# Optimization experiments

Measured on AMD Instinct MI355X. Metric: run time of the kernel, lower is better.

## Reference

```python
import jax, jax.numpy as jnp
import numpy as np

LN_EPS = 1e-5

def _proj(x, w, b):
    # 1x1 conv: x [B,C,H,W], w [O,C], b [O]
    return jnp.einsum('bchw,oc->bohw', x, w) + b[None, :, None, None]

def _layernorm(x, w, b):
    # normalize over last dim
    mu = jnp.mean(x, axis=-1, keepdims=True)
    var = jnp.mean(jnp.square(x - mu), axis=-1, keepdims=True)
    return (x - mu) * jax.lax.rsqrt(var + LN_EPS) * w + b

def setup_inputs() -> dict:
    key = jax.random.key(0)
    ks = jax.random.split(key, 12)
    C = 256
    d = {
        's3': jax.random.normal(ks[0], (2, C, 64, 64), jnp.float32),
        's4': jax.random.normal(ks[1], (2, C, 32, 64), jnp.float32),
        's5': jax.random.normal(ks[2], (2, C, 16, 64), jnp.float32),
        'qw': jax.random.normal(ks[3], (C, C), jnp.float32) * 0.02,
        'qb': jax.random.normal(ks[4], (C,), jnp.float32) * 0.02,
        'kw': jax.random.normal(ks[5], (C, C), jnp.float32) * 0.02,
        'kb': jax.random.normal(ks[6], (C,), jnp.float32) * 0.02,
        'vw': jax.random.normal(ks[7], (C, C), jnp.float32) * 0.02,
        'vb': jax.random.normal(ks[8], (C,), jnp.float32) * 0.02,
        'ow': jax.random.normal(ks[9], (C, C), jnp.float32) * 0.02,
        'ob': jax.random.normal(ks[10], (C,), jnp.float32) * 0.02,
        'ln_w': jnp.ones((C,), jnp.float32),
        'ln_b': jnp.zeros((C,), jnp.float32),
    }
    return d

def reference(s3, s4, s5, qw, qb, kw, kb, vw, vb, ow, ob, ln_w, ln_b):
    B, C, H, W = s3.shape
    num_heads = 8
    head_dim = C // num_heads
    scale = head_dim ** -0.5

    q = _proj(s3, qw, qb).reshape(B, C, H * W)            # [B,C,Nq]
    k4 = _proj(s4, kw, kb).reshape(B, C, -1)
    k5 = _proj(s5, kw, kb).reshape(B, C, -1)
    v4 = _proj(s4, vw, vb).reshape(B, C, -1)
    v5 = _proj(s5, vw, vb).reshape(B, C, -1)
    k = jnp.concatenate([k4, k5], axis=-1)                # [B,C,Nk]
    v = jnp.concatenate([v4, v5], axis=-1)

    # [B,C,N] -> [B,h,N,d]
    def split_heads(t):
        Bn, Cn, N = t.shape
        return t.transpose(0, 2, 1).reshape(Bn, N, num_heads, head_dim).transpose(0, 2, 1, 3)

    qh, kh, vh = split_heads(q), split_heads(k), split_heads(v)
    attn = jnp.einsum('bhqd,bhkd->bhqk', qh, kh) * scale
    attn = jax.nn.softmax(attn, axis=-1)
    out = jnp.einsum('bhqk,bhkd->bhqd', attn, vh)         # [B,h,Nq,d]
    out = out.transpose(0, 2, 1, 3).reshape(B, H * W, C)  # [B,Nq,C]
    out = out.transpose(0, 2, 1).reshape(B, C, H, W)
    out = _proj(out, ow, ob)
    out = s3 + out
    out_flat = out.reshape(B, C, H * W).transpose(0, 2, 1)  # [B,N,C]
    out_flat = _layernorm(out_flat, ln_w, ln_b)
    return out_flat.transpose(0, 2, 1).reshape(B, C, H, W)
```

## Files before the change

kernel.cpp:

```cpp
#include <hip/hip_runtime.h>

typedef __bf16 bf16;
typedef __bf16 bf16x4 __attribute__((ext_vector_type(4)));
typedef __bf16 bf16x8 __attribute__((ext_vector_type(8)));
typedef _Float16 f16;
typedef _Float16 f16x2 __attribute__((ext_vector_type(2)));
typedef _Float16 f16x4 __attribute__((ext_vector_type(4)));
typedef _Float16 f16x8 __attribute__((ext_vector_type(8)));
typedef float f32x4 __attribute__((ext_vector_type(4)));
typedef unsigned int u32x4 __attribute__((ext_vector_type(4)));

#define MFMA16 __builtin_amdgcn_mfma_f32_16x16x32_bf16
#define MFMA16H __builtin_amdgcn_mfma_f32_16x16x32_f16

__device__ __forceinline__ void async16(void* lds, const void* g) {
    __builtin_amdgcn_global_load_lds((const __attribute__((address_space(1))) unsigned int*)g,
                                     (__attribute__((address_space(3))) unsigned int*)lds, 16, 0, 0);
}

__device__ __forceinline__ f16x2 pkrtz(float a, float b) {
    return __builtin_bit_cast(f16x2, __builtin_amdgcn_cvt_pkrtz(a, b));
}

__device__ __forceinline__ float fdot2h(f16x2 a, f16x2 b, float c) {
#if __has_builtin(__builtin_amdgcn_fdot2)
    return __builtin_amdgcn_fdot2(a, b, c, false);
#else
    return c + (float)a[0] * (float)b[0] + (float)a[1] * (float)b[1];
#endif
}

__global__ __launch_bounds__(256) void k_prep(const float* __restrict__ qw, const float* __restrict__ kw,
                                              const float* __restrict__ vw, const float* __restrict__ ow,
                                              bf16* __restrict__ Wb,
                                              const float* __restrict__ s3, const float* __restrict__ s4,
                                              const float* __restrict__ s5,
                                              bf16* __restrict__ s3t, bf16* __restrict__ s45t) {
    __shared__ float T[64][65];
    int bx = blockIdx.x, t = threadIdx.x;
    if (bx < 256) {
        int tt = bx * 256 + t;
        const float* srcs[4] = {qw, kw, vw, ow};
        int which = tt >> 14;
        int idx = (tt & 16383) * 4;
        f32x4 v = *(const f32x4*)(srcs[which] + idx);
        bf16x4 o;
        o[0] = (bf16)v[0]; o[1] = (bf16)v[1]; o[2] = (bf16)v[2]; o[3] = (bf16)v[3];
        *(bf16x4*)(Wb + (size_t)which * 65536 + idx) = o;
        return;
    }
    const float* src; bf16* dst; int N, dstRows, rowOff, x, y, z;
    if (bx < 768)       { int i = bx - 256;  src = s3; dst = s3t;  N = 4096; dstRows = 4096; rowOff = 0;    x = i & 63; y = (i >> 6) & 3; z = i >> 8; }
    else if (bx < 1024) { int i = bx - 768;  src = s4; dst = s45t; N = 2048; dstRows = 3072; rowOff = 0;    x = i & 31; y = (i >> 5) & 3; z = i >> 7; }
    else                { int i = bx - 1024; src = s5; dst = s45t; N = 1024; dstRows = 3072; rowOff = 2048; x = i & 15; y = (i >> 4) & 3; z = i >> 6; }
    int c0 = y * 64, n0 = x * 64, b = z;
    const float* s = src + ((size_t)b * 256 + c0) * N + n0;
#pragma unroll
    for (int i = 0; i < 4; i++) {
        int flat = i * 256 + t;
        int row = flat >> 4;
        int col = (flat & 15) * 4;
        f32x4 v = *(const f32x4*)(s + (size_t)row * N + col);
        T[row][col + 0] = v[0]; T[row][col + 1] = v[1];
        T[row][col + 2] = v[2]; T[row][col + 3] = v[3];
    }
    __syncthreads();
#pragma unroll
    for (int i = 0; i < 4; i++) {
        int flat = i * 256 + t;
        int nrow = flat >> 4;
        int c4 = (flat & 15) * 4;
        bf16x4 o;
        o[0] = (bf16)T[c4 + 0][nrow]; o[1] = (bf16)T[c4 + 1][nrow];
        o[2] = (bf16)T[c4 + 2][nrow]; o[3] = (bf16)T[c4 + 3][nrow];
        *(bf16x4*)(dst + ((size_t)(b * dstRows + rowOff + n0 + nrow)) * 256 + c0 + c4) = o;
    }
}

__global__ __launch_bounds__(256) void k_qkv(const bf16* __restrict__ Wb,
                                             const bf16* __restrict__ s3t, const bf16* __restrict__ s45t,
                                             const float* __restrict__ qb, const float* __restrict__ kb,
                                             const float* __restrict__ vb,
                                             bf16* __restrict__ Qb, bf16* __restrict__ Kb,
                                             f16* __restrict__ Vtb, float qscale) {
    int i = blockIdx.x;
    int mode, n0, m0, b, Nrows;
    const bf16 *A, *Bt; const float* bias; float oscale = 1.0f;
    if (i < 512) {
        mode = 0; A = Wb; Bt = s3t; bias = qb; Nrows = 4096; oscale = qscale;
        n0 = (i & 63) * 64; m0 = ((i >> 6) & 3) * 64; b = i >> 8;
    } else if (i < 896) {
        unsigned j = i - 512;
        mode = 1; A = Wb + 65536; Bt = s45t; bias = kb; Nrows = 3072;
        n0 = (j % 48u) * 64; unsigned rr = j / 48u; m0 = (rr & 3) * 64; b = rr >> 2;
    } else {
        unsigned j = i - 896;
        mode = 2; A = Wb + 131072; Bt = s45t; bias = vb; Nrows = 3072;
        n0 = (j % 48u) * 64; unsigned rr = j / 48u; m0 = (rr & 3) * 64; b = rr >> 2;
    }
    __shared__ bf16 As[64 * 40];
    __shared__ bf16 Bs[64 * 40];
    int t = threadIdx.x;
    int w = t >> 6, lane = t & 63;
    int lrow = lane & 15, lk = lane >> 4;
    f32x4 acc[4] = {};
    int r = t >> 2, cc = (t & 3) * 8;
    for (int kc = 0; kc < 256; kc += 32) {
        u32x4 va = *(const u32x4*)(A + (size_t)(m0 + r) * 256 + kc + cc);
        u32x4 vbv = *(const u32x4*)(Bt + ((size_t)b * Nrows + n0 + r) * 256 + kc + cc);
        *(u32x4*)(As + r * 40 + cc) = va;
        *(u32x4*)(Bs + r * 40 + cc) = vbv;
        __syncthreads();
        bf16x8 af = *(const bf16x8*)(As + (w * 16 + lrow) * 40 + lk * 8);
#pragma unroll
        for (int ct = 0; ct < 4; ct++) {
            bf16x8 bfr = *(const bf16x8*)(Bs + (ct * 16 + lrow) * 40 + lk * 8);
            acc[ct] = MFMA16(af, bfr, acc[ct], 0, 0, 0);
        }
        __syncthreads();
    }
    int o0 = m0 + w * 16 + lk * 4;
    f32x4 b4 = *(const f32x4*)(bias + o0);
    int head = o0 >> 5;
#pragma unroll
    for (int ct = 0; ct < 4; ct++) {
        int n = n0 + ct * 16 + lrow;
        if (mode == 0) {
            int dd = o0 & 31;
            bf16x4 pv;
#pragma unroll
            for (int j = 0; j < 4; j++) pv[j] = (bf16)((acc[ct][j] + b4[j]) * oscale);
            *(bf16x4*)(Qb + ((size_t)(b * 8 + head) * 4096 + n) * 32 + dd) = pv;
        } else if (mode == 1) {
            int dd = o0 & 31;
            int u = n & 31;
            int np = (n & ~31) | (((u >> 2) & 1) << 4) | ((u >> 3) << 2) | (u & 3);
            bf16x4 pv;
#pragma unroll
            for (int j = 0; j < 4; j++) pv[j] = (bf16)(acc[ct][j] + b4[j]);
            *(bf16x4*)(Kb + ((size_t)(b * 8 + head) * 3072 + np) * 32 + dd) = pv;
        } else {
            int g = (n & 63) >> 3;
#pragma unroll
            for (int j = 0; j < 4; j++) {
                int dd = (o0 & 31) + j;
                int col = (n & ~63) + ((g ^ (dd & 7)) << 3) + (n & 7);
                Vtb[((size_t)(b * 8 + head) * 32 + dd) * 3072 + col] = (f16)(acc[ct][j] + b4[j]);
            }
        }
    }
}

__global__ __launch_bounds__(256, 4) void k_attn(const bf16* __restrict__ Q, const bf16* __restrict__ K,
                                                 const f16* __restrict__ Vt,
                                                 f16* __restrict__ Opart, float* __restrict__ Lsum) {
    int bh = blockIdx.y;
    int q0 = blockIdx.x * 128;
    int sp = blockIdx.z;
    int kn0 = sp * 768;
    int t = threadIdx.x, w = t >> 6, lane = t & 63;
    int lrow = lane & 15, lk = lane >> 4;
    __shared__ __align__(16) char smem[16896];
    bf16* Ks = (bf16*)smem;
    f16* Vs = (f16*)(smem + 8192);
    f16* Tq = (f16*)smem;
    const bf16* kbase = K + (size_t)bh * 3072 * 32;
    const f16* vbase = Vt + (size_t)bh * 32 * 3072;
    const bf16* kg = kbase + (size_t)(kn0 + w * 16 + (lane >> 2)) * 32 + (lane & 3) * 8;
    const f16* vg = vbase + (size_t)(w * 8 + (lane >> 3)) * 3072 + kn0 + (lane & 7) * 8;
    bf16x8 aq[2];
#pragma unroll
    for (int qg = 0; qg < 2; ++qg)
        aq[qg] = *(const bf16x8*)(Q + ((size_t)bh * 4096 + q0 + w * 32 + qg * 16 + lrow) * 32 + lk * 8);
    f32x4 accO[2][2] = {};
    float lsum[2] = {0.f, 0.f};
    f32x4 zero = {};
    f16x2 one2; one2[0] = (f16)1.f; one2[1] = (f16)1.f;
    int vkey = lrow & 7;
    async16(Ks + w * 512, kg);
    async16(Vs + w * 512, vg);
    __syncthreads();
    for (int c = 0; c < 12; ++c) {
        int buf = c & 1;
        if (c < 11) {
            async16(Ks + (buf ^ 1) * 2048 + w * 512, kg + (size_t)(c + 1) * 64 * 32);
            async16(Vs + (buf ^ 1) * 2048 + w * 512, vg + (c + 1) * 64);
        }
        const bf16* ksb = Ks + buf * 2048;
        const f16* vsb = Vs + buf * 2048;
#pragma unroll
        for (int p = 0; p < 2; ++p) {
            f32x4 s[2][2];
#pragma unroll
            for (int t2 = 0; t2 < 2; ++t2) {
                bf16x8 kf = *(const bf16x8*)(ksb + (p * 32 + t2 * 16 + lrow) * 32 + lk * 8);
#pragma unroll
                for (int qg = 0; qg < 2; ++qg) s[t2][qg] = MFMA16(kf, aq[qg], zero, 0, 0, 0);
            }
            f16x8 vf0 = *(const f16x8*)(vsb + lrow * 64 + ((((p << 2) | lk) ^ vkey) << 3));
            f16x8 vf1 = *(const f16x8*)(vsb + (16 + lrow) * 64 + ((((p << 2) | lk) ^ vkey) << 3));
#pragma unroll
            for (int qg = 0; qg < 2; ++qg) {
                f16x2 h0 = pkrtz(__builtin_amdgcn_exp2f(s[0][qg][0]), __builtin_amdgcn_exp2f(s[0][qg][1]));
                f16x2 h1 = pkrtz(__builtin_amdgcn_exp2f(s[0][qg][2]), __builtin_amdgcn_exp2f(s[0][qg][3]));
                f16x2 h2 = pkrtz(__builtin_amdgcn_exp2f(s[1][qg][0]), __builtin_amdgcn_exp2f(s[1][qg][1]));
                f16x2 h3 = pkrtz(__builtin_amdgcn_exp2f(s[1][qg][2]), __builtin_amdgcn_exp2f(s[1][qg][3]));
                f16x8 pk;
                pk[0] = h0[0]; pk[1] = h0[1]; pk[2] = h1[0]; pk[3] = h1[1];
                pk[4] = h2[0]; pk[5] = h2[1]; pk[6] = h3[0]; pk[7] = h3[1];
                lsum[qg] = fdot2h(h0, one2, lsum[qg]);
                lsum[qg] = fdot2h(h1, one2, lsum[qg]);
                lsum[qg] = fdot2h(h2, one2, lsum[qg]);
                lsum[qg] = fdot2h(h3, one2, lsum[qg]);
                accO[qg][0] = MFMA16H(vf0, pk, accO[qg][0], 0, 0, 0);
                accO[qg][1] = MFMA16H(vf1, pk, accO[qg][1], 0, 0, 0);
            }
        }
        __syncthreads();
    }
    int sb = sp * 16 + bh;
#pragma unroll
    for (int qg = 0; qg < 2; ++qg) {
        lsum[qg] += __shfl_xor(lsum[qg], 16, 64);
        lsum[qg] += __shfl_xor(lsum[qg], 32, 64);
    }
    if (lane < 16) {
#pragma unroll
        for (int qg = 0; qg < 2; ++qg)
            Lsum[(size_t)sb * 4096 + q0 + w * 32 + qg * 16 + lane] = lsum[qg];
    }
    f16* tw = Tq + w * 1088;
#pragma unroll
    for (int qg = 0; qg < 2; ++qg)
#pragma unroll
        for (int dh = 0; dh < 2; ++dh)
#pragma unroll
            for (int i = 0; i < 4; ++i)
                tw[(dh * 16 + lk * 4 + i) * 34 + qg * 16 + lrow] = (f16)accO[qg][dh][i];
    int q2 = (lane & 15) * 2, dgrp = (lane >> 4) * 8;
#pragma unroll
    for (int qq = 0; qq < 2; ++qq) {
        f16x8 ov;
#pragma unroll
        for (int dj = 0; dj < 8; ++dj) ov[dj] = tw[(dgrp + dj) * 34 + q2 + qq];
        *(f16x8*)(Opart + ((size_t)sb * 4096 + q0 + w * 32 + q2 + qq) * 32 + dgrp) = ov;
    }
}

__global__ __launch_bounds__(256) void k_oln(const bf16* __restrict__ A, const f16* __restrict__ Opart,
                                             const float* __restrict__ Ls, const float* __restrict__ bias,
                                             const bf16* __restrict__ s3t,
                                             const float* __restrict__ lnw, const float* __restrict__ lnb,
                                             float* __restrict__ out) {
    int i = blockIdx.x;
    int b = i >> 7, n0 = (i & 127) * 32;
    __shared__ __align__(16) char smem[34176];
    bf16* As = (bf16*)smem;
    bf16* Bs = (bf16*)(smem + 20480);
    float* T = (float*)smem;
    float* ps = (float*)(smem + 32896);
    float* pq = (float*)(smem + 33408);
    float* mu_s = (float*)(smem + 33920);
    float* rs_s = (float*)(smem + 34048);
    int t = threadIdx.x, w = t >> 6, lane = t & 63;
    int lrow = lane & 15, lk = lane >> 4;
    f32x4 acc[4][2] = {};
    int rB = t >> 3, cgB = (t & 7) * 4;
    int q = n0 + rB;
    const size_t SPS = (size_t)16 * 4096 * 32;
    for (int kc = 0; kc < 256; kc += 32) {
        int bh = b * 8 + (kc >> 5);
        const bf16* ar = A + (size_t)t * 256 + kc;
        u32x4 va0 = *(const u32x4*)(ar);
        u32x4 va1 = *(const u32x4*)(ar + 8);
        u32x4 va2 = *(const u32x4*)(ar + 16);
        u32x4 va3 = *(const u32x4*)(ar + 24);
        float l = 0.f;
#pragma unroll
        for (int sp = 0; sp < 4; ++sp) l += Ls[(size_t)(sp * 16 + bh) * 4096 + q];
        float rl = 1.0f / l;
        const f16* obp = Opart + ((size_t)bh * 4096 + q) * 32 + cgB;
        f32x4 sv = {};
#pragma unroll
        for (int sp = 0; sp < 4; ++sp) {
            f16x4 av = *(const f16x4*)(obp + sp * SPS);
#pragma unroll
            for (int j = 0; j < 4; ++j) sv[j] += (float)av[j];
        }
        bf16x4 bb;
#pragma unroll
        for (int j = 0; j < 4; ++j) bb[j] = (bf16)(sv[j] * rl);
        *(u32x4*)(As + t * 40 + 0) = va0;
        *(u32x4*)(As + t * 40 + 8) = va1;
        *(u32x4*)(As + t * 40 + 16) = va2;
        *(u32x4*)(As + t * 40 + 24) = va3;
        *(bf16x4*)(Bs + rB * 40 + cgB) = bb;
        __syncthreads();
#pragma unroll
        for (int mt = 0; mt < 4; ++mt) {
            bf16x8 af = *(const bf16x8*)(As + (mt * 64 + w * 16 + lrow) * 40 + lk * 8);
#pragma unroll
            for (int ct = 0; ct < 2; ++ct) {
                bf16x8 bfr = *(const bf16x8*)(Bs + (ct * 16 + lrow) * 40 + lk * 8);
                acc[mt][ct] = MFMA16(af, bfr, acc[mt][ct], 0, 0, 0);
            }
        }
        __syncthreads();
    }
    float wsum[2] = {0.f, 0.f}, wsq[2] = {0.f, 0.f};
#pragma unroll
    for (int ct = 0; ct < 2; ++ct) {
        int n = ct * 16 + lrow;
#pragma unroll
        for (int mt = 0; mt < 4; ++mt) {
            int c0 = mt * 64 + w * 16 + lk * 4;
            f32x4 b4 = *(const f32x4*)(bias + c0);
            bf16x4 rv = *(const bf16x4*)(s3t + ((size_t)b * 4096 + n0 + n) * 256 + c0);
#pragma unroll
            for (int j = 0; j < 4; ++j) {
                float v = acc[mt][ct][j] + b4[j] + (float)rv[j];
                T[n * 257 + c0 + j] = v;
                wsum[ct] += v;
                wsq[ct] += v * v;
            }
        }
    }
#pragma unroll
    for (int ct = 0; ct < 2; ++ct) {
        wsum[ct] += __shfl_xor(wsum[ct], 16, 64);
        wsum[ct] += __shfl_xor(wsum[ct], 32, 64);
        wsq[ct] += __shfl_xor(wsq[ct], 16, 64);
        wsq[ct] += __shfl_xor(wsq[ct], 32, 64);
    }
    if (lk == 0) {
#pragma unroll
        for (int ct = 0; ct < 2; ++ct) {
            ps[w * 32 + ct * 16 + lrow] = wsum[ct];
            pq[w * 32 + ct * 16 + lrow] = wsq[ct];
        }
    }
    __syncthreads();
    if (t < 32) {
        float S = ps[t] + ps[32 + t] + ps[64 + t] + ps[96 + t];
        float Q2 = pq[t] + pq[32 + t] + pq[64 + t] + pq[96 + t];
        float m = S * (1.0f / 256.0f);
        mu_s[t] = m;
        rs_s[t] = rsqrtf(Q2 * (1.0f / 256.0f) - m * m + 1e-5f);
    }
    __syncthreads();
    int cb = t >> 3, n4 = (t & 7) * 4;
#pragma unroll
    for (int cc8 = 0; cc8 < 8; ++cc8) {
        int c = cb + cc8 * 32;
        float wv = lnw[c], bv = lnb[c];
        f32x4 o;
#pragma unroll
        for (int k2 = 0; k2 < 4; ++k2)
            o[k2] = (T[(n4 + k2) * 257 + c] - mu_s[n4 + k2]) * rs_s[n4 + k2] * wv + bv;
        *(f32x4*)(out + ((size_t)b * 256 + c) * 4096 + n0 + n4) = o;
    }
}

extern "C" void kernel_launch(void* const* d_in, const int* in_sizes, int n_in,
                              void* d_out, int out_size, void* d_ws, size_t ws_size,
                              hipStream_t stream) {
    const float* s3  = (const float*)d_in[0];
    const float* s4  = (const float*)d_in[1];
    const float* s5  = (const float*)d_in[2];
    const float* qw  = (const float*)d_in[3];
    const float* qb  = (const float*)d_in[4];
    const float* kw  = (const float*)d_in[5];
    const float* kb  = (const float*)d_in[6];
    const float* vw  = (const float*)d_in[7];
    const float* vb  = (const float*)d_in[8];
    const float* ow  = (const float*)d_in[9];
    const float* ob  = (const float*)d_in[10];
    const float* lnw = (const float*)d_in[11];
    const float* lnb = (const float*)d_in[12];
    float* out = (float*)d_out;
    char* ws = (char*)d_ws;

    bf16* Wb    = (bf16*)(ws);
    bf16* s3t   = (bf16*)(ws + (512ull << 10));
    bf16* s45t  = (bf16*)(ws + (4608ull << 10));
    bf16* Qb    = (bf16*)(ws + (7680ull << 10));
    bf16* Kb    = Qb + (2ull * 8 * 4096 * 32);
    f16*  Vtb   = (f16*)(Kb + (2ull * 8 * 3072 * 32));
    f16*  Opart = (f16*)(ws + (17920ull << 10));
    float* Lsum = (float*)(ws + (34304ull << 10));

    const float qscale = 0.17677669529663688f * 1.4426950408889634f;

    k_prep<<<1152, 256, 0, stream>>>(qw, kw, vw, ow, Wb, s3, s4, s5, s3t, s45t);
    k_qkv<<<1280, 256, 0, stream>>>(Wb, s3t, s45t, qb, kb, vb, Qb, Kb, Vtb, qscale);
    k_attn<<<dim3(32, 16, 4), 256, 0, stream>>>(Qb, Kb, Vtb, Opart, Lsum);
    k_oln<<<256, 256, 0, stream>>>(Wb + 196608, Opart, Lsum, ob, s3t, lnw, lnb, out);
}
```

Baseline: 145.0 us.

## Halve attention key splits, swizzle K LDS reads, and shrink out-proj tile

```diff
diff --git a/kernel.cpp b/kernel.cpp
--- a/kernel.cpp
+++ b/kernel.cpp
@@ -157,7 +157,7 @@
     int bh = blockIdx.y;
     int q0 = blockIdx.x * 128;
     int sp = blockIdx.z;
-    int kn0 = sp * 768;
+    int kn0 = sp * 1536;
     int t = threadIdx.x, w = t >> 6, lane = t & 63;
     int lrow = lane & 15, lk = lane >> 4;
     __shared__ __align__(16) char smem[16896];
@@ -166,7 +166,8 @@
     f16* Tq = (f16*)smem;
     const bf16* kbase = K + (size_t)bh * 3072 * 32;
     const f16* vbase = Vt + (size_t)bh * 32 * 3072;
-    const bf16* kg = kbase + (size_t)(kn0 + w * 16 + (lane >> 2)) * 32 + (lane & 3) * 8;
+    const bf16* kg = kbase + (size_t)(kn0 + w * 16 + (lane >> 2)) * 32
+                           + (((lane & 3) ^ ((lane >> 3) & 3)) << 3);
     const f16* vg = vbase + (size_t)(w * 8 + (lane >> 3)) * 3072 + kn0 + (lane & 7) * 8;
     bf16x8 aq[2];
 #pragma unroll
@@ -177,12 +178,13 @@
     f32x4 zero = {};
     f16x2 one2; one2[0] = (f16)1.f; one2[1] = (f16)1.f;
     int vkey = lrow & 7;
+    int kkey = (lrow >> 1) & 3;
     async16(Ks + w * 512, kg);
     async16(Vs + w * 512, vg);
     __syncthreads();
-    for (int c = 0; c < 12; ++c) {
+    for (int c = 0; c < 24; ++c) {
         int buf = c & 1;
-        if (c < 11) {
+        if (c < 23) {
             async16(Ks + (buf ^ 1) * 2048 + w * 512, kg + (size_t)(c + 1) * 64 * 32);
             async16(Vs + (buf ^ 1) * 2048 + w * 512, vg + (c + 1) * 64);
         }
@@ -193,7 +195,7 @@
             f32x4 s[2][2];
 #pragma unroll
             for (int t2 = 0; t2 < 2; ++t2) {
-                bf16x8 kf = *(const bf16x8*)(ksb + (p * 32 + t2 * 16 + lrow) * 32 + lk * 8);
+                bf16x8 kf = *(const bf16x8*)(ksb + (p * 32 + t2 * 16 + lrow) * 32 + ((lk ^ kkey) << 3));
 #pragma unroll
                 for (int qg = 0; qg < 2; ++qg) s[t2][qg] = MFMA16(kf, aq[qg], zero, 0, 0, 0);
             }
@@ -253,19 +255,19 @@
                                              const float* __restrict__ lnw, const float* __restrict__ lnb,
                                              float* __restrict__ out) {
     int i = blockIdx.x;
-    int b = i >> 7, n0 = (i & 127) * 32;
-    __shared__ __align__(16) char smem[34176];
+    int b = i >> 8, n0 = (i & 255) * 16;
+    __shared__ __align__(16) char smem[21760];
     bf16* As = (bf16*)smem;
     bf16* Bs = (bf16*)(smem + 20480);
     float* T = (float*)smem;
-    float* ps = (float*)(smem + 32896);
-    float* pq = (float*)(smem + 33408);
-    float* mu_s = (float*)(smem + 33920);
-    float* rs_s = (float*)(smem + 34048);
+    float* ps = (float*)(smem + 16448);
+    float* pq = (float*)(smem + 16704);
+    float* mu_s = (float*)(smem + 16960);
+    float* rs_s = (float*)(smem + 17024);
     int t = threadIdx.x, w = t >> 6, lane = t & 63;
     int lrow = lane & 15, lk = lane >> 4;
-    f32x4 acc[4][2] = {};
-    int rB = t >> 3, cgB = (t & 7) * 4;
+    f32x4 acc[4] = {};
+    int rB = (t >> 3) & 15, cgB = (t & 7) * 4;
     int q = n0 + rB;
     const size_t SPS = (size_t)16 * 4096 * 32;
     for (int kc = 0; kc < 256; kc += 32) {
@@ -275,83 +277,66 @@
         u32x4 va1 = *(const u32x4*)(ar + 8);
         u32x4 va2 = *(const u32x4*)(ar + 16);
         u32x4 va3 = *(const u32x4*)(ar + 24);
-        float l = 0.f;
-#pragma unroll
-        for (int sp = 0; sp < 4; ++sp) l += Ls[(size_t)(sp * 16 + bh) * 4096 + q];
-        float rl = 1.0f / l;
-        const f16* obp = Opart + ((size_t)bh * 4096 + q) * 32 + cgB;
-        f32x4 sv = {};
-#pragma unroll
-        for (int sp = 0; sp < 4; ++sp) {
-            f16x4 av = *(const f16x4*)(obp + sp * SPS);
-#pragma unroll
-            for (int j = 0; j < 4; ++j) sv[j] += (float)av[j];
-        }
-        bf16x4 bb;
-#pragma unroll
-        for (int j = 0; j < 4; ++j) bb[j] = (bf16)(sv[j] * rl);
         *(u32x4*)(As + t * 40 + 0) = va0;
         *(u32x4*)(As + t * 40 + 8) = va1;
         *(u32x4*)(As + t * 40 + 16) = va2;
         *(u32x4*)(As + t * 40 + 24) = va3;
-        *(bf16x4*)(Bs + rB * 40 + cgB) = bb;
-        __syncthreads();
+        if (t < 128) {
+            float l = Ls[(size_t)bh * 4096 + q] + Ls[(size_t)(16 + bh) * 4096 + q];
+            float rl = 1.0f / l;
+            const f16* obp = Opart + ((size_t)bh * 4096 + q) * 32 + cgB;
+            f16x4 a0 = *(const f16x4*)(obp);
+            f16x4 a1 = *(const f16x4*)(obp + SPS);
+            bf16x4 bb;
+#pragma unroll
+            for (int j = 0; j < 4; ++j) bb[j] = (bf16)(((float)a0[j] + (float)a1[j]) * rl);
+            *(bf16x4*)(Bs + rB * 40 + cgB) = bb;
+        }
+        __syncthreads();
+        bf16x8 bfr = *(const bf16x8*)(Bs + lrow * 40 + lk * 8);
 #pragma unroll
         for (int mt = 0; mt < 4; ++mt) {
             bf16x8 af = *(const bf16x8*)(As + (mt * 64 + w * 16 + lrow) * 40 + lk * 8);
-#pragma unroll
-            for (int ct = 0; ct < 2; ++ct) {
-                bf16x8 bfr = *(const bf16x8*)(Bs + (ct * 16 + lrow) * 40 + lk * 8);
-                acc[mt][ct] = MFMA16(af, bfr, acc[mt][ct], 0, 0, 0);
-            }
-        }
-        __syncthreads();
-    }
-    float wsum[2] = {0.f, 0.f}, wsq[2] = {0.f, 0.f};
-#pragma unroll
-    for (int ct = 0; ct < 2; ++ct) {
-        int n = ct * 16 + lrow;
-#pragma unroll
-        for (int mt = 0; mt < 4; ++mt) {
-            int c0 = mt * 64 + w * 16 + lk * 4;
-            f32x4 b4 = *(const f32x4*)(bias + c0);
-            bf16x4 rv = *(const bf16x4*)(s3t + ((size_t)b * 4096 + n0 + n) * 256 + c0);
-#pragma unroll
-            for (int j = 0; j < 4; ++j) {
-                float v = acc[mt][ct][j] + b4[j] + (float)rv[j];
-                T[n * 257 + c0 + j] = v;
-                wsum[ct] += v;
-                wsq[ct] += v * v;
-            }
-        }
-    }
-#pragma unroll
-    for (int ct = 0; ct < 2; ++ct) {
-        wsum[ct] += __shfl_xor(wsum[ct], 16, 64);
-        wsum[ct] += __shfl_xor(wsum[ct], 32, 64);
-        wsq[ct] += __shfl_xor(wsq[ct], 16, 64);
-        wsq[ct] += __shfl_xor(wsq[ct], 32, 64);
-    }
+            acc[mt] = MFMA16(af, bfr, acc[mt], 0, 0, 0);
+        }
+        __syncthreads();
+    }
+    float wsum = 0.f, wsq = 0.f;
+    int n = lrow;
+#pragma unroll
+    for (int mt = 0; mt < 4; ++mt) {
+        int c0 = mt * 64 + w * 16 + lk * 4;
+        f32x4 b4 = *(const f32x4*)(bias + c0);
+        bf16x4 rv = *(const bf16x4*)(s3t + ((size_t)b * 4096 + n0 + n) * 256 + c0);
+#pragma unroll
+        for (int j = 0; j < 4; ++j) {
+            float v = acc[mt][j] + b4[j] + (float)rv[j];
+            T[n * 257 + c0 + j] = v;
+            wsum += v;
+            wsq += v * v;
+        }
+    }
+    wsum += __shfl_xor(wsum, 16, 64);
+    wsum += __shfl_xor(wsum, 32, 64);
+    wsq += __shfl_xor(wsq, 16, 64);
+    wsq += __shfl_xor(wsq, 32, 64);
     if (lk == 0) {
-#pragma unroll
-        for (int ct = 0; ct < 2; ++ct) {
-            ps[w * 32 + ct * 16 + lrow] = wsum[ct];
-            pq[w * 32 + ct * 16 + lrow] = wsq[ct];
-        }
+        ps[w * 16 + lrow] = wsum;
+        pq[w * 16 + lrow] = wsq;
     }
     __syncthreads();
-    if (t < 32) {
-        float S = ps[t] + ps[32 + t] + ps[64 + t] + ps[96 + t];
-        float Q2 = pq[t] + pq[32 + t] + pq[64 + t] + pq[96 + t];
+    if (t < 16) {
+        float S = ps[t] + ps[16 + t] + ps[32 + t] + ps[48 + t];
+        float Q2 = pq[t] + pq[16 + t] + pq[32 + t] + pq[48 + t];
         float m = S * (1.0f / 256.0f);
         mu_s[t] = m;
         rs_s[t] = rsqrtf(Q2 * (1.0f / 256.0f) - m * m + 1e-5f);
     }
     __syncthreads();
-    int cb = t >> 3, n4 = (t & 7) * 4;
-#pragma unroll
-    for (int cc8 = 0; cc8 < 8; ++cc8) {
-        int c = cb + cc8 * 32;
+    int cb = t >> 2, n4 = (t & 3) * 4;
+#pragma unroll
+    for (int cc4 = 0; cc4 < 4; ++cc4) {
+        int c = cb + cc4 * 64;
         float wv = lnw[c], bv = lnb[c];
         f32x4 o;
 #pragma unroll
@@ -393,6 +378,6 @@
 
     k_prep<<<1152, 256, 0, stream>>>(qw, kw, vw, ow, Wb, s3, s4, s5, s3t, s45t);
     k_qkv<<<1280, 256, 0, stream>>>(Wb, s3t, s45t, qb, kb, vb, Qb, Kb, Vtb, qscale);
-    k_attn<<<dim3(32, 16, 4), 256, 0, stream>>>(Qb, Kb, Vtb, Opart, Lsum);
-    k_oln<<<256, 256, 0, stream>>>(Wb + 196608, Opart, Lsum, ob, s3t, lnw, lnb, out);
-}
+    k_attn<<<dim3(32, 16, 2), 256, 0, stream>>>(Qb, Kb, Vtb, Opart, Lsum);
+    k_oln<<<512, 256, 0, stream>>>(Wb + 196608, Opart, Lsum, ob, s3t, lnw, lnb, out);
+}
```

Measured after the change: 151.5 us. 4.5% more time.

## Double-buffer QKV GEMM with async LDS loads and halve attention key splits

Applied to the files above, without the earlier changes.

```diff
diff --git a/kernel.cpp b/kernel.cpp
--- a/kernel.cpp
+++ b/kernel.cpp
@@ -98,23 +98,27 @@
         mode = 2; A = Wb + 131072; Bt = s45t; bias = vb; Nrows = 3072;
         n0 = (j % 48u) * 64; unsigned rr = j / 48u; m0 = (rr & 3) * 64; b = rr >> 2;
     }
-    __shared__ bf16 As[64 * 40];
-    __shared__ bf16 Bs[64 * 40];
+    __shared__ __align__(16) bf16 As[2][64 * 32];
+    __shared__ __align__(16) bf16 Bs[2][64 * 32];
     int t = threadIdx.x;
     int w = t >> 6, lane = t & 63;
     int lrow = lane & 15, lk = lane >> 4;
     f32x4 acc[4] = {};
-    int r = t >> 2, cc = (t & 3) * 8;
-    for (int kc = 0; kc < 256; kc += 32) {
-        u32x4 va = *(const u32x4*)(A + (size_t)(m0 + r) * 256 + kc + cc);
-        u32x4 vbv = *(const u32x4*)(Bt + ((size_t)b * Nrows + n0 + r) * 256 + kc + cc);
-        *(u32x4*)(As + r * 40 + cc) = va;
-        *(u32x4*)(Bs + r * 40 + cc) = vbv;
-        __syncthreads();
-        bf16x8 af = *(const bf16x8*)(As + (w * 16 + lrow) * 40 + lk * 8);
+    const bf16* Ag = A + (size_t)(m0 + w * 16 + (lane >> 2)) * 256 + (lane & 3) * 8;
+    const bf16* Bg = Bt + ((size_t)b * Nrows + n0 + w * 16 + (lane >> 2)) * 256 + (lane & 3) * 8;
+    async16(&As[0][w * 512], Ag);
+    async16(&Bs[0][w * 512], Bg);
+    __syncthreads();
+    for (int s8 = 0; s8 < 8; ++s8) {
+        int buf = s8 & 1;
+        if (s8 < 7) {
+            async16(&As[buf ^ 1][w * 512], Ag + (s8 + 1) * 32);
+            async16(&Bs[buf ^ 1][w * 512], Bg + (s8 + 1) * 32);
+        }
+        bf16x8 af = *(const bf16x8*)(&As[buf][(w * 16 + lrow) * 32 + lk * 8]);
 #pragma unroll
         for (int ct = 0; ct < 4; ct++) {
-            bf16x8 bfr = *(const bf16x8*)(Bs + (ct * 16 + lrow) * 40 + lk * 8);
+            bf16x8 bfr = *(const bf16x8*)(&Bs[buf][(ct * 16 + lrow) * 32 + lk * 8]);
             acc[ct] = MFMA16(af, bfr, acc[ct], 0, 0, 0);
         }
         __syncthreads();
@@ -157,7 +161,7 @@
     int bh = blockIdx.y;
     int q0 = blockIdx.x * 128;
     int sp = blockIdx.z;
-    int kn0 = sp * 768;
+    int kn0 = sp * 1536;
     int t = threadIdx.x, w = t >> 6, lane = t & 63;
     int lrow = lane & 15, lk = lane >> 4;
     __shared__ __align__(16) char smem[16896];
@@ -180,9 +184,9 @@
     async16(Ks + w * 512, kg);
     async16(Vs + w * 512, vg);
     __syncthreads();
-    for (int c = 0; c < 12; ++c) {
+    for (int c = 0; c < 24; ++c) {
         int buf = c & 1;
-        if (c < 11) {
+        if (c < 23) {
             async16(Ks + (buf ^ 1) * 2048 + w * 512, kg + (size_t)(c + 1) * 64 * 32);
             async16(Vs + (buf ^ 1) * 2048 + w * 512, vg + (c + 1) * 64);
         }
@@ -275,21 +279,14 @@
         u32x4 va1 = *(const u32x4*)(ar + 8);
         u32x4 va2 = *(const u32x4*)(ar + 16);
         u32x4 va3 = *(const u32x4*)(ar + 24);
-        float l = 0.f;
-#pragma unroll
-        for (int sp = 0; sp < 4; ++sp) l += Ls[(size_t)(sp * 16 + bh) * 4096 + q];
+        float l = Ls[(size_t)bh * 4096 + q] + Ls[(size_t)(16 + bh) * 4096 + q];
         float rl = 1.0f / l;
         const f16* obp = Opart + ((size_t)bh * 4096 + q) * 32 + cgB;
-        f32x4 sv = {};
-#pragma unroll
-        for (int sp = 0; sp < 4; ++sp) {
-            f16x4 av = *(const f16x4*)(obp + sp * SPS);
-#pragma unroll
-            for (int j = 0; j < 4; ++j) sv[j] += (float)av[j];
-        }
+        f16x4 a0 = *(const f16x4*)(obp);
+        f16x4 a1 = *(const f16x4*)(obp + SPS);
         bf16x4 bb;
 #pragma unroll
-        for (int j = 0; j < 4; ++j) bb[j] = (bf16)(sv[j] * rl);
+        for (int j = 0; j < 4; ++j) bb[j] = (bf16)(((float)a0[j] + (float)a1[j]) * rl);
         *(u32x4*)(As + t * 40 + 0) = va0;
         *(u32x4*)(As + t * 40 + 8) = va1;
         *(u32x4*)(As + t * 40 + 16) = va2;
@@ -393,6 +390,6 @@
 
     k_prep<<<1152, 256, 0, stream>>>(qw, kw, vw, ow, Wb, s3, s4, s5, s3t, s45t);
     k_qkv<<<1280, 256, 0, stream>>>(Wb, s3t, s45t, qb, kb, vb, Qb, Kb, Vtb, qscale);
-    k_attn<<<dim3(32, 16, 4), 256, 0, stream>>>(Qb, Kb, Vtb, Opart, Lsum);
+    k_attn<<<dim3(32, 16, 2), 256, 0, stream>>>(Qb, Kb, Vtb, Opart, Lsum);
     k_oln<<<256, 256, 0, stream>>>(Wb + 196608, Opart, Lsum, ob, s3t, lnw, lnb, out);
 }
```

After: 148.0 us. 2.1% more time.
